# Performance work log

Measured on AMD Instinct MI355X. Metric: run time of the kernel, lower is better.

Reference implementation:

```python
import jax, jax.numpy as jnp
import numpy as np

ALPHA = 0.5        # damping from conf['alpha']
MAX_ITERS = 30     # fixed-point iterations (conf uses up to 150 with eps early-exit)
GN_GROUPS = 3
GN_EPS = 1e-5
SLOPE = 0.01       # F.leaky_relu default negative_slope


def _conv(x, w, b, pad):
    y = jax.lax.conv_general_dilated(
        x, w, window_strides=(1, 1), padding=[(pad, pad), (pad, pad)],
        dimension_numbers=("NCHW", "OIHW", "NCHW"))
    return y + b[None, :, None, None]


def _leaky(x):
    return jnp.where(x >= 0, x, SLOPE * x)


def _groupnorm(x, gamma, beta):
    N, C, H, W = x.shape
    xg = x.reshape(N, GN_GROUPS, C // GN_GROUPS, H, W)
    mu = xg.mean(axis=(2, 3, 4), keepdims=True)
    var = xg.var(axis=(2, 3, 4), keepdims=True)
    xg = (xg - mu) * jax.lax.rsqrt(var + GN_EPS)
    x = xg.reshape(N, C, H, W)
    return x * gamma[None, :, None, None] + beta[None, :, None, None]


def setup_inputs() -> dict:
    key = jax.random.key(0)
    ks = jax.random.split(key, 8)
    image = jax.random.normal(ks[0], (1024, 3, 32, 32), dtype=jnp.float32)
    # Unit params (small init keeps the fixed-point iteration contractive)
    w1 = jax.random.normal(ks[1], (6, 8, 5, 5), dtype=jnp.float32) * 0.05
    b1 = jnp.zeros((6,), jnp.float32)
    gamma = jnp.ones((6,), jnp.float32)
    beta = jnp.zeros((6,), jnp.float32)
    w2 = jax.random.normal(ks[2], (5, 6, 5, 5), dtype=jnp.float32) * 0.05
    b2 = jnp.zeros((5,), jnp.float32)
    # detection head: Conv2d(5, 10, 32, padding=0) -> full-image conv
    wh = jax.random.normal(ks[3], (10, 5, 32, 32), dtype=jnp.float32) * 0.01
    bh = jnp.zeros((10,), jnp.float32)
    return {"image": image, "w1": w1, "b1": b1, "gamma": gamma, "beta": beta,
            "w2": w2, "b2": b2, "wh": wh, "bh": bh}


def reference(image, w1, b1, gamma, beta, w2, b2, wh, bh):
    N = image.shape[0]
    z0 = jnp.zeros((N, 5, 32, 32), image.dtype)

    def unit(z):
        zx = jnp.concatenate([z, image], axis=1)
        h = _groupnorm(_leaky(_conv(zx, w1, b1, 2)), gamma, beta)
        return _leaky(_conv(h, w2, b2, 2))

    def step(z, _):
        z = (1.0 - ALPHA) * z + ALPHA * unit(z)
        return z, None

    z, _ = jax.lax.scan(step, z0, None, length=MAX_ITERS)
    return _conv(z, wh, bh, 0)
```

## Files before the change

kernel.cpp:

```cpp
#include <hip/hip_runtime.h>
#include <hip/hip_fp16.h>


typedef _Float16 half8 __attribute__((ext_vector_type(8)));
typedef float f32x4 __attribute__((ext_vector_type(4)));

#define HOFF   34
#define NBUF   (71 * 36 * 4)
#define WL1_DW 10224
#define WL2_DW 12784
#define NLDS   15344

__device__ __forceinline__ unsigned pk2(float a, float b) {
    __half2 h = __float22half2_rn(make_float2(a, b));
    return *reinterpret_cast<unsigned*>(&h);
}
__device__ __forceinline__ float2 up2(unsigned u) {
    __half2 h = *reinterpret_cast<__half2*>(&u);
    return __half22float2(h);
}
__device__ __forceinline__ unsigned hmul2(unsigned a, unsigned b) {
    __half2 r = __hmul2(*reinterpret_cast<__half2*>(&a), *reinterpret_cast<__half2*>(&b));
    return *reinterpret_cast<unsigned*>(&r);
}
__device__ __forceinline__ float lrelu(float x) { return fmaxf(x, 0.01f * x); }
__device__ __forceinline__ int swz(int x) { return (x * 16) ^ ((x & 8) << 1); }
__device__ __forceinline__ int bofs(int r, int x) { return r * 576 + swz(x); }

__global__ void pack_weights(const float* __restrict__ w1,
                             const float* __restrict__ w2,
                             unsigned* __restrict__ ws)
{
    int t = blockIdx.x * 256 + threadIdx.x;
    if (t < 640) {
        int c = t >> 6, l = t & 63;
        int row = l & 15, tg = l >> 4;
        int dx = row >> 3, oc = row & 7;
        int ty = c >> 1, tx = 4 * (c & 1) + tg, kx = tx - dx;
        unsigned q[4];
        #pragma unroll
        for (int d = 0; d < 4; ++d) {
            float v0 = 0.f, v1 = 0.f;
            if (oc < 6 && kx >= 0 && kx < 5) {
                v0 = w1[(oc * 8 + 2 * d) * 25 + ty * 5 + kx];
                v1 = w1[(oc * 8 + 2 * d + 1) * 25 + ty * 5 + kx];
            }
            q[d] = pk2(v0, v1);
        }
        *(uint4*)&ws[t * 4] = make_uint4(q[0], q[1], q[2], q[3]);
    } else if (t < 1280) {
        int u = t - 640;
        int c = u >> 6, l = u & 63;
        int row = l & 15, tg = l >> 4;
        int dx = row >> 3, oc = row & 7;
        int ty = c >> 1, tx = 4 * (c & 1) + tg, kx = tx - dx;
        unsigned q[4];
        #pragma unroll
        for (int d = 0; d < 4; ++d) {
            float v0 = 0.f, v1 = 0.f;
            if (oc < 5 && kx >= 0 && kx < 5) {
                if (2 * d < 6)     v0 = w2[(oc * 6 + 2 * d) * 25 + ty * 5 + kx];
                if (2 * d + 1 < 6) v1 = w2[(oc * 6 + 2 * d + 1) * 25 + ty * 5 + kx];
            }
            q[d] = pk2(v0, v1);
        }
        *(uint4*)&ws[2560 + u * 4] = make_uint4(q[0], q[1], q[2], q[3]);
    }
}

__global__ __launch_bounds__(256, 2)
void deq_kernel(const float* __restrict__ image,
                const unsigned* __restrict__ wks,
                const float* __restrict__ b1,
                const float* __restrict__ gam, const float* __restrict__ bet,
                const float* __restrict__ b2,
                const float* __restrict__ wh, const float* __restrict__ bh,
                float* __restrict__ out)
{
    __shared__ __align__(16) unsigned lds[NLDS];
    __shared__ float red[48];

    const int n    = blockIdx.x;
    const int tid  = threadIdx.x;
    const int lane = tid & 63;
    const int wid  = tid >> 6;
    const int col  = lane & 15;
    const int tg   = lane >> 4;
    const int dxl  = tg >> 1;
    const int sub  = tg & 1;

    for (int p = tid; p < NBUF; p += 256) lds[p] = 0u;
    for (int p = tid; p < 2560; p += 256) {
        lds[WL1_DW + p] = wks[p];
        lds[WL2_DW + p] = wks[2560 + p];
    }
    __syncthreads();

    {
        const int yy = tid >> 3, xx0 = (tid & 7) << 2;
        float4 i0 = *(const float4*)&image[(n * 3 + 0) * 1024 + yy * 32 + xx0];
        float4 i1 = *(const float4*)&image[(n * 3 + 1) * 1024 + yy * 32 + xx0];
        float4 i2 = *(const float4*)&image[(n * 3 + 2) * 1024 + yy * 32 + xx0];
        float a0[4] = {i0.x, i0.y, i0.z, i0.w};
        float a1[4] = {i1.x, i1.y, i1.z, i1.w};
        float a2[4] = {i2.x, i2.y, i2.z, i2.w};
        #pragma unroll
        for (int i = 0; i < 4; ++i) {
            unsigned* bp = (unsigned*)((char*)lds + bofs(yy + 2, xx0 + 2 + i));
            bp[2] = pk2(0.f, a0[i]);
            bp[3] = pk2(a1[i], a2[i]);
            unsigned* hp = (unsigned*)((char*)lds + bofs(yy + 2 + HOFF, xx0 + 2 + i));
            hp[3] = 0x00003C00u;
        }
    }

    int sx2[2];
    #pragma unroll
    for (int txh = 0; txh < 2; ++txh)
        sx2[txh] = swz(2 * col + 4 * txh + tg);

    float b1q[4], b2q[4];
    #pragma unroll
    for (int r = 0; r < 4; ++r) {
        int oc = (tg * 4 + r) & 7;
        b1q[r] = (oc < 6) ? b1[oc] : 0.f;
        b2q[r] = (oc < 5) ? b2[oc] : 0.f;
    }
    const f32x4 ai1 = {b1q[0], b1q[1], b1q[2], b1q[3]};
    const f32x4 ai2 = {b2q[0], b2q[1], b2q[2], b2q[3]};

    __syncthreads();

    const int ay0 = wid << 3;
    const int hwB = bofs(0, 2 * col + dxl + 2);
    const int wlo = lane << 2;

    #pragma unroll 1
    for (int it = 0; it < 30; ++it) {
        uint4 fw[10];
        #pragma unroll
        for (int c = 0; c < 10; ++c)
            fw[c] = *(const uint4*)&lds[WL1_DW + c * 256 + wlo];

        f32x4 acc[8];
        #pragma unroll
        for (int g = 0; g < 8; ++g) acc[g] = ai1;

        #pragma unroll
        for (int pr = 0; pr < 12; ++pr) {
            const char* rowp = (const char*)lds + (ay0 + pr) * 576;
            #pragma unroll
            for (int txh = 0; txh < 2; ++txh) {
                half8 pv = *(const half8*)(rowp + sx2[txh]);
                #pragma unroll
                for (int ty = 0; ty < 5; ++ty) {
                    const int g = pr - ty;
                    if (g >= 0 && g < 8)
                        acc[g] = __builtin_amdgcn_mfma_f32_16x16x32_f16(
                            __builtin_bit_cast(half8, fw[ty * 2 + txh]), pv, acc[g], 0, 0, 0);
                }
            }
        }

        float ps_lo = 0.f, ps_hi = 0.f, pq_lo = 0.f, pq_hi = 0.f;
        #pragma unroll
        for (int g = 0; g < 8; ++g) {
            float h0 = lrelu(acc[g][0]), h1 = lrelu(acc[g][1]);
            float h2 = lrelu(acc[g][2]), h3 = lrelu(acc[g][3]);
            ps_lo += h0 + h1;  pq_lo = fmaf(h0, h0, fmaf(h1, h1, pq_lo));
            ps_hi += h2 + h3;  pq_hi = fmaf(h2, h2, fmaf(h3, h3, pq_hi));
            char* wp = (char*)lds + (ay0 + g + 2 + HOFF) * 576 + (hwB - 0 * 576);
            wp = (char*)lds + bofs(ay0 + g + 2 + HOFF, 2 * col + dxl + 2);
            if (sub == 0) {
                *(uint2*)wp = make_uint2(pk2(h0, h1), pk2(h2, h3));
            } else {
                *(unsigned*)(wp + 8) = pk2(h0, h1);
            }
        }

        #pragma unroll
        for (int m = 1; m <= 8; m <<= 1) {
            ps_lo += __shfl_xor(ps_lo, m); ps_hi += __shfl_xor(ps_hi, m);
            pq_lo += __shfl_xor(pq_lo, m); pq_hi += __shfl_xor(pq_hi, m);
        }
        ps_lo += __shfl_xor(ps_lo, 32); ps_hi += __shfl_xor(ps_hi, 32);
        pq_lo += __shfl_xor(pq_lo, 32); pq_hi += __shfl_xor(pq_hi, 32);
        if (lane == 0)  { red[wid * 8 + 0] = ps_lo; red[wid * 8 + 1] = ps_hi;
                          red[wid * 8 + 4] = pq_lo; red[wid * 8 + 5] = pq_hi; }
        if (lane == 16) { red[wid * 8 + 2] = ps_lo; red[wid * 8 + 6] = pq_lo; }
        __syncthreads();

        float scv[6], shv[6];
        #pragma unroll
        for (int g3 = 0; g3 < 3; ++g3) {
            float s = 0.f, q = 0.f;
            #pragma unroll
            for (int w = 0; w < 4; ++w) { s += red[w * 8 + g3]; q += red[w * 8 + 4 + g3]; }
            float mean = s * (1.f / 2048.f);
            float var  = q * (1.f / 2048.f) - mean * mean;
            float inv  = rsqrtf(var + 1e-5f);
            #pragma unroll
            for (int k = 0; k < 2; ++k) {
                int c = 2 * g3 + k;
                scv[c] = inv * gam[c];
                shv[c] = bet[c] - mean * scv[c];
            }
        }
        unsigned sp0 = pk2(scv[0], scv[1]), sp1 = pk2(scv[2], scv[3]), sp2 = pk2(scv[4], scv[5]);

        #pragma unroll
        for (int c = 0; c < 10; ++c) {
            uint4 wr = *(const uint4*)&lds[WL2_DW + c * 256 + wlo];
            float2 a = up2(wr.x), b = up2(wr.y), cc = up2(wr.z);
            float pw = fmaf(a.x, shv[0], fmaf(a.y, shv[1],
                       fmaf(b.x, shv[2], fmaf(b.y, shv[3],
                       fmaf(cc.x, shv[4], cc.y * shv[5])))));
            fw[c].x = hmul2(wr.x, sp0);
            fw[c].y = hmul2(wr.y, sp1);
            fw[c].z = hmul2(wr.z, sp2);
            fw[c].w = pk2(pw, 0.f);
        }

        #pragma unroll
        for (int g = 0; g < 8; ++g) acc[g] = ai2;

        #pragma unroll
        for (int pr = 0; pr < 12; ++pr) {
            const char* rowp = (const char*)lds + (HOFF + ay0 + pr) * 576;
            #pragma unroll
            for (int txh = 0; txh < 2; ++txh) {
                half8 pv = *(const half8*)(rowp + sx2[txh]);
                #pragma unroll
                for (int ty = 0; ty < 5; ++ty) {
                    const int g = pr - ty;
                    if (g >= 0 && g < 8)
                        acc[g] = __builtin_amdgcn_mfma_f32_16x16x32_f16(
                            __builtin_bit_cast(half8, fw[ty * 2 + txh]), pv, acc[g], 0, 0, 0);
                }
            }
        }

        #pragma unroll
        for (int g = 0; g < 8; ++g) {
            char* zp = (char*)lds + bofs(ay0 + g + 2, 2 * col + dxl + 2);
            if (sub == 0) {
                uint2 zo = *(uint2*)zp;
                float2 za = up2(zo.x), zc = up2(zo.y);
                float z0 = 0.5f * za.x + 0.5f * lrelu(acc[g][0]);
                float z1 = 0.5f * za.y + 0.5f * lrelu(acc[g][1]);
                float z2 = 0.5f * zc.x + 0.5f * lrelu(acc[g][2]);
                float z3 = 0.5f * zc.y + 0.5f * lrelu(acc[g][3]);
                *(uint2*)zp = make_uint2(pk2(z0, z1), pk2(z2, z3));
            } else {
                _Float16* pz = (_Float16*)(zp + 8);
                float z4 = 0.5f * (float)pz[0] + 0.5f * lrelu(acc[g][0]);
                pz[0] = (_Float16)z4;
            }
        }
        __syncthreads();
    }

    {
        const int yy = tid >> 3, xx0 = (tid & 7) << 2;
        float zf[5][4];
        #pragma unroll
        for (int i = 0; i < 4; ++i) {
            const unsigned* bp = (const unsigned*)((const char*)lds + bofs(yy + 2, xx0 + 2 + i));
            float2 f0 = up2(bp[0]), fb = up2(bp[1]), fc = up2(bp[2]);
            zf[0][i] = f0.x; zf[1][i] = f0.y; zf[2][i] = fb.x; zf[3][i] = fb.y; zf[4][i] = fc.x;
        }
        float ho[10];
        #pragma unroll
        for (int o = 0; o < 10; ++o) ho[o] = 0.f;
        #pragma unroll
        for (int c = 0; c < 5; ++c) {
            #pragma unroll
            for (int o = 0; o < 10; ++o) {
                float4 wv = *(const float4*)&wh[(o * 5 + c) * 1024 + yy * 32 + xx0];
                ho[o] = fmaf(zf[c][0], wv.x, ho[o]);
                ho[o] = fmaf(zf[c][1], wv.y, ho[o]);
                ho[o] = fmaf(zf[c][2], wv.z, ho[o]);
                ho[o] = fmaf(zf[c][3], wv.w, ho[o]);
            }
        }
        #pragma unroll
        for (int m = 1; m < 64; m <<= 1) {
            #pragma unroll
            for (int o = 0; o < 10; ++o) ho[o] += __shfl_xor(ho[o], m);
        }
        if (lane == 0) {
            #pragma unroll
            for (int o = 0; o < 10; ++o) red[wid * 10 + o] = ho[o];
        }
    }
    __syncthreads();
    if (tid < 10)
        out[n * 10 + tid] = red[tid] + red[10 + tid] + red[20 + tid] + red[30 + tid] + bh[tid];
}

extern "C" void kernel_launch(void* const* d_in, const int* in_sizes, int n_in,
                              void* d_out, int out_size, void* d_ws, size_t ws_size,
                              hipStream_t stream) {
    const float* image = (const float*)d_in[0];
    const float* w1    = (const float*)d_in[1];
    const float* b1    = (const float*)d_in[2];
    const float* gam   = (const float*)d_in[3];
    const float* bet   = (const float*)d_in[4];
    const float* w2    = (const float*)d_in[5];
    const float* b2    = (const float*)d_in[6];
    const float* wh    = (const float*)d_in[7];
    const float* bh    = (const float*)d_in[8];
    float* out = (float*)d_out;
    unsigned* ws = (unsigned*)d_ws;

    pack_weights<<<5, 256, 0, stream>>>(w1, w2, ws);

    const int N = in_sizes[0] / (3 * 32 * 32);
    deq_kernel<<<N, 256, 0, stream>>>(image, ws, b1, gam, bet, b2, wh, bh, out);
}
```

Before: 335.8 us.

## Process each image with a single wavefront and keep conv weights in registers

Each image is now handled by one 64-thread wavefront instead of four, looping over four 8-row bands in series. This removes all block barriers and the shared-memory reduction for the group-norm statistics, which now use wave shuffles. Both packed conv weight sets are held in registers rather than reloaded from LDS every iteration, which also shrinks LDS per block. The trade-off is far fewer waves resident per CU, so MFMA and LDS latency are less hidden, and each image takes longer on its own.

```diff
diff --git a/kernel.cpp b/kernel.cpp
--- a/kernel.cpp
+++ b/kernel.cpp
@@ -5,11 +5,8 @@
 typedef _Float16 half8 __attribute__((ext_vector_type(8)));
 typedef float f32x4 __attribute__((ext_vector_type(4)));
 
-#define HOFF   34
-#define NBUF   (71 * 36 * 4)
-#define WL1_DW 10224
-#define WL2_DW 12784
-#define NLDS   15344
+#define HOFF 34
+#define NBUF (71 * 36 * 4)
 
 __device__ __forceinline__ unsigned pk2(float a, float b) {
     __half2 h = __float22half2_rn(make_float2(a, b));
@@ -68,7 +65,7 @@
     }
 }
 
-__global__ __launch_bounds__(256, 2)
+__global__ __launch_bounds__(64, 1)
 void deq_kernel(const float* __restrict__ image,
                 const unsigned* __restrict__ wks,
                 const float* __restrict__ b1,
@@ -77,41 +74,45 @@
                 const float* __restrict__ wh, const float* __restrict__ bh,
                 float* __restrict__ out)
 {
-    __shared__ __align__(16) unsigned lds[NLDS];
-    __shared__ float red[48];
+    __shared__ __align__(16) unsigned lds[NBUF];
 
     const int n    = blockIdx.x;
-    const int tid  = threadIdx.x;
-    const int lane = tid & 63;
-    const int wid  = tid >> 6;
+    const int lane = threadIdx.x;
     const int col  = lane & 15;
     const int tg   = lane >> 4;
     const int dxl  = tg >> 1;
     const int sub  = tg & 1;
 
-    for (int p = tid; p < NBUF; p += 256) lds[p] = 0u;
-    for (int p = tid; p < 2560; p += 256) {
-        lds[WL1_DW + p] = wks[p];
-        lds[WL2_DW + p] = wks[2560 + p];
-    }
+    for (int p = lane; p < NBUF; p += 64) lds[p] = 0u;
     __syncthreads();
 
     {
-        const int yy = tid >> 3, xx0 = (tid & 7) << 2;
-        float4 i0 = *(const float4*)&image[(n * 3 + 0) * 1024 + yy * 32 + xx0];
-        float4 i1 = *(const float4*)&image[(n * 3 + 1) * 1024 + yy * 32 + xx0];
-        float4 i2 = *(const float4*)&image[(n * 3 + 2) * 1024 + yy * 32 + xx0];
-        float a0[4] = {i0.x, i0.y, i0.z, i0.w};
-        float a1[4] = {i1.x, i1.y, i1.z, i1.w};
-        float a2[4] = {i2.x, i2.y, i2.z, i2.w};
-        #pragma unroll
-        for (int i = 0; i < 4; ++i) {
-            unsigned* bp = (unsigned*)((char*)lds + bofs(yy + 2, xx0 + 2 + i));
-            bp[2] = pk2(0.f, a0[i]);
-            bp[3] = pk2(a1[i], a2[i]);
-            unsigned* hp = (unsigned*)((char*)lds + bofs(yy + 2 + HOFF, xx0 + 2 + i));
-            hp[3] = 0x00003C00u;
-        }
+        #pragma unroll 1
+        for (int r = 0; r < 4; ++r) {
+            int t = lane + r * 64;
+            const int yy = t >> 3, xx0 = (t & 7) << 2;
+            float4 i0 = *(const float4*)&image[(n * 3 + 0) * 1024 + yy * 32 + xx0];
+            float4 i1 = *(const float4*)&image[(n * 3 + 1) * 1024 + yy * 32 + xx0];
+            float4 i2 = *(const float4*)&image[(n * 3 + 2) * 1024 + yy * 32 + xx0];
+            float a0[4] = {i0.x, i0.y, i0.z, i0.w};
+            float a1[4] = {i1.x, i1.y, i1.z, i1.w};
+            float a2[4] = {i2.x, i2.y, i2.z, i2.w};
+            #pragma unroll
+            for (int i = 0; i < 4; ++i) {
+                unsigned* bp = (unsigned*)((char*)lds + bofs(yy + 2, xx0 + 2 + i));
+                bp[2] = pk2(0.f, a0[i]);
+                bp[3] = pk2(a1[i], a2[i]);
+                unsigned* hp = (unsigned*)((char*)lds + bofs(yy + 2 + HOFF, xx0 + 2 + i));
+                hp[3] = 0x00003C00u;
+            }
+        }
+    }
+
+    uint4 f1[10], f2[10];
+    #pragma unroll
+    for (int c = 0; c < 10; ++c) {
+        f1[c] = *(const uint4*)&wks[(c * 64 + lane) * 4];
+        f2[c] = *(const uint4*)&wks[2560 + (c * 64 + lane) * 4];
     }
 
     int sx2[2];
@@ -119,62 +120,60 @@
     for (int txh = 0; txh < 2; ++txh)
         sx2[txh] = swz(2 * col + 4 * txh + tg);
 
+    const int chb = sub * 4;
     float b1q[4], b2q[4];
     #pragma unroll
     for (int r = 0; r < 4; ++r) {
-        int oc = (tg * 4 + r) & 7;
+        int oc = chb + r;
         b1q[r] = (oc < 6) ? b1[oc] : 0.f;
         b2q[r] = (oc < 5) ? b2[oc] : 0.f;
     }
     const f32x4 ai1 = {b1q[0], b1q[1], b1q[2], b1q[3]};
     const f32x4 ai2 = {b2q[0], b2q[1], b2q[2], b2q[3]};
+    float gv[6], bv[6];
+    #pragma unroll
+    for (int c = 0; c < 6; ++c) { gv[c] = gam[c]; bv[c] = bet[c]; }
 
     __syncthreads();
 
-    const int ay0 = wid << 3;
-    const int hwB = bofs(0, 2 * col + dxl + 2);
-    const int wlo = lane << 2;
+    const int hwx = swz(2 * col + dxl + 2);
 
     #pragma unroll 1
     for (int it = 0; it < 30; ++it) {
-        uint4 fw[10];
-        #pragma unroll
-        for (int c = 0; c < 10; ++c)
-            fw[c] = *(const uint4*)&lds[WL1_DW + c * 256 + wlo];
-
-        f32x4 acc[8];
-        #pragma unroll
-        for (int g = 0; g < 8; ++g) acc[g] = ai1;
-
-        #pragma unroll
-        for (int pr = 0; pr < 12; ++pr) {
-            const char* rowp = (const char*)lds + (ay0 + pr) * 576;
-            #pragma unroll
-            for (int txh = 0; txh < 2; ++txh) {
-                half8 pv = *(const half8*)(rowp + sx2[txh]);
+        float ps_lo = 0.f, ps_hi = 0.f, pq_lo = 0.f, pq_hi = 0.f;
+        #pragma unroll 1
+        for (int b = 0; b < 4; ++b) {
+            const int ay = b << 3;
+            f32x4 acc[8];
+            #pragma unroll
+            for (int g = 0; g < 8; ++g) acc[g] = ai1;
+            #pragma unroll
+            for (int pr = 0; pr < 12; ++pr) {
+                const char* rowp = (const char*)lds + (ay + pr) * 576;
                 #pragma unroll
-                for (int ty = 0; ty < 5; ++ty) {
-                    const int g = pr - ty;
-                    if (g >= 0 && g < 8)
-                        acc[g] = __builtin_amdgcn_mfma_f32_16x16x32_f16(
-                            __builtin_bit_cast(half8, fw[ty * 2 + txh]), pv, acc[g], 0, 0, 0);
-                }
-            }
-        }
-
-        float ps_lo = 0.f, ps_hi = 0.f, pq_lo = 0.f, pq_hi = 0.f;
-        #pragma unroll
-        for (int g = 0; g < 8; ++g) {
-            float h0 = lrelu(acc[g][0]), h1 = lrelu(acc[g][1]);
-            float h2 = lrelu(acc[g][2]), h3 = lrelu(acc[g][3]);
-            ps_lo += h0 + h1;  pq_lo = fmaf(h0, h0, fmaf(h1, h1, pq_lo));
-            ps_hi += h2 + h3;  pq_hi = fmaf(h2, h2, fmaf(h3, h3, pq_hi));
-            char* wp = (char*)lds + (ay0 + g + 2 + HOFF) * 576 + (hwB - 0 * 576);
-            wp = (char*)lds + bofs(ay0 + g + 2 + HOFF, 2 * col + dxl + 2);
-            if (sub == 0) {
-                *(uint2*)wp = make_uint2(pk2(h0, h1), pk2(h2, h3));
-            } else {
-                *(unsigned*)(wp + 8) = pk2(h0, h1);
+                for (int txh = 0; txh < 2; ++txh) {
+                    half8 pv = *(const half8*)(rowp + sx2[txh]);
+                    #pragma unroll
+                    for (int ty = 0; ty < 5; ++ty) {
+                        const int g = pr - ty;
+                        if (g >= 0 && g < 8)
+                            acc[g] = __builtin_amdgcn_mfma_f32_16x16x32_f16(
+                                __builtin_bit_cast(half8, f1[ty * 2 + txh]), pv, acc[g], 0, 0, 0);
+                    }
+                }
+            }
+            #pragma unroll
+            for (int g = 0; g < 8; ++g) {
+                float h0 = lrelu(acc[g][0]), h1 = lrelu(acc[g][1]);
+                float h2 = lrelu(acc[g][2]), h3 = lrelu(acc[g][3]);
+                ps_lo += h0 + h1;  pq_lo = fmaf(h0, h0, fmaf(h1, h1, pq_lo));
+                ps_hi += h2 + h3;  pq_hi = fmaf(h2, h2, fmaf(h3, h3, pq_hi));
+                char* wp = (char*)lds + (ay + g + 2 + HOFF) * 576 + hwx;
+                if (sub == 0) {
+                    *(uint2*)wp = make_uint2(pk2(h0, h1), pk2(h2, h3));
+                } else {
+                    *(unsigned*)(wp + 8) = pk2(h0, h1);
+                }
             }
         }
 
@@ -185,102 +184,105 @@
         }
         ps_lo += __shfl_xor(ps_lo, 32); ps_hi += __shfl_xor(ps_hi, 32);
         pq_lo += __shfl_xor(pq_lo, 32); pq_hi += __shfl_xor(pq_hi, 32);
-        if (lane == 0)  { red[wid * 8 + 0] = ps_lo; red[wid * 8 + 1] = ps_hi;
-                          red[wid * 8 + 4] = pq_lo; red[wid * 8 + 5] = pq_hi; }
-        if (lane == 16) { red[wid * 8 + 2] = ps_lo; red[wid * 8 + 6] = pq_lo; }
-        __syncthreads();
+        float sg[3], qg[3];
+        sg[0] = __shfl(ps_lo, 0);  qg[0] = __shfl(pq_lo, 0);
+        sg[1] = __shfl(ps_hi, 0);  qg[1] = __shfl(pq_hi, 0);
+        sg[2] = __shfl(ps_lo, 16); qg[2] = __shfl(pq_lo, 16);
 
         float scv[6], shv[6];
         #pragma unroll
         for (int g3 = 0; g3 < 3; ++g3) {
-            float s = 0.f, q = 0.f;
-            #pragma unroll
-            for (int w = 0; w < 4; ++w) { s += red[w * 8 + g3]; q += red[w * 8 + 4 + g3]; }
-            float mean = s * (1.f / 2048.f);
-            float var  = q * (1.f / 2048.f) - mean * mean;
+            float mean = sg[g3] * (1.f / 2048.f);
+            float var  = qg[g3] * (1.f / 2048.f) - mean * mean;
             float inv  = rsqrtf(var + 1e-5f);
             #pragma unroll
             for (int k = 0; k < 2; ++k) {
                 int c = 2 * g3 + k;
-                scv[c] = inv * gam[c];
-                shv[c] = bet[c] - mean * scv[c];
+                scv[c] = inv * gv[c];
+                shv[c] = bv[c] - mean * scv[c];
             }
         }
         unsigned sp0 = pk2(scv[0], scv[1]), sp1 = pk2(scv[2], scv[3]), sp2 = pk2(scv[4], scv[5]);
 
+        uint4 fw[10];
         #pragma unroll
         for (int c = 0; c < 10; ++c) {
-            uint4 wr = *(const uint4*)&lds[WL2_DW + c * 256 + wlo];
-            float2 a = up2(wr.x), b = up2(wr.y), cc = up2(wr.z);
+            float2 a = up2(f2[c].x), bb = up2(f2[c].y), cc = up2(f2[c].z);
             float pw = fmaf(a.x, shv[0], fmaf(a.y, shv[1],
-                       fmaf(b.x, shv[2], fmaf(b.y, shv[3],
+                       fmaf(bb.x, shv[2], fmaf(bb.y, shv[3],
                        fmaf(cc.x, shv[4], cc.y * shv[5])))));
-            fw[c].x = hmul2(wr.x, sp0);
-            fw[c].y = hmul2(wr.y, sp1);
-            fw[c].z = hmul2(wr.z, sp2);
+            fw[c].x = hmul2(f2[c].x, sp0);
+            fw[c].y = hmul2(f2[c].y, sp1);
+            fw[c].z = hmul2(f2[c].z, sp2);
             fw[c].w = pk2(pw, 0.f);
         }
 
-        #pragma unroll
-        for (int g = 0; g < 8; ++g) acc[g] = ai2;
-
-        #pragma unroll
-        for (int pr = 0; pr < 12; ++pr) {
-            const char* rowp = (const char*)lds + (HOFF + ay0 + pr) * 576;
-            #pragma unroll
-            for (int txh = 0; txh < 2; ++txh) {
-                half8 pv = *(const half8*)(rowp + sx2[txh]);
+        #pragma unroll 1
+        for (int b = 0; b < 4; ++b) {
+            const int ay = b << 3;
+            f32x4 acc[8];
+            #pragma unroll
+            for (int g = 0; g < 8; ++g) acc[g] = ai2;
+            #pragma unroll
+            for (int pr = 0; pr < 12; ++pr) {
+                const char* rowp = (const char*)lds + (HOFF + ay + pr) * 576;
                 #pragma unroll
-                for (int ty = 0; ty < 5; ++ty) {
-                    const int g = pr - ty;
-                    if (g >= 0 && g < 8)
-                        acc[g] = __builtin_amdgcn_mfma_f32_16x16x32_f16(
-                            __builtin_bit_cast(half8, fw[ty * 2 + txh]), pv, acc[g], 0, 0, 0);
-                }
-            }
-        }
-
-        #pragma unroll
-        for (int g = 0; g < 8; ++g) {
-            char* zp = (char*)lds + bofs(ay0 + g + 2, 2 * col + dxl + 2);
-            if (sub == 0) {
-                uint2 zo = *(uint2*)zp;
-                float2 za = up2(zo.x), zc = up2(zo.y);
-                float z0 = 0.5f * za.x + 0.5f * lrelu(acc[g][0]);
-                float z1 = 0.5f * za.y + 0.5f * lrelu(acc[g][1]);
-                float z2 = 0.5f * zc.x + 0.5f * lrelu(acc[g][2]);
-                float z3 = 0.5f * zc.y + 0.5f * lrelu(acc[g][3]);
-                *(uint2*)zp = make_uint2(pk2(z0, z1), pk2(z2, z3));
-            } else {
-                _Float16* pz = (_Float16*)(zp + 8);
-                float z4 = 0.5f * (float)pz[0] + 0.5f * lrelu(acc[g][0]);
-                pz[0] = (_Float16)z4;
-            }
-        }
-        __syncthreads();
+                for (int txh = 0; txh < 2; ++txh) {
+                    half8 pv = *(const half8*)(rowp + sx2[txh]);
+                    #pragma unroll
+                    for (int ty = 0; ty < 5; ++ty) {
+                        const int g = pr - ty;
+                        if (g >= 0 && g < 8)
+                            acc[g] = __builtin_amdgcn_mfma_f32_16x16x32_f16(
+                                __builtin_bit_cast(half8, fw[ty * 2 + txh]), pv, acc[g], 0, 0, 0);
+                    }
+                }
+            }
+            #pragma unroll
+            for (int g = 0; g < 8; ++g) {
+                char* zp = (char*)lds + (ay + g + 2) * 576 + hwx;
+                if (sub == 0) {
+                    uint2 zo = *(uint2*)zp;
+                    float2 za = up2(zo.x), zc = up2(zo.y);
+                    float z0 = 0.5f * za.x + 0.5f * lrelu(acc[g][0]);
+                    float z1 = 0.5f * za.y + 0.5f * lrelu(acc[g][1]);
+                    float z2 = 0.5f * zc.x + 0.5f * lrelu(acc[g][2]);
+                    float z3 = 0.5f * zc.y + 0.5f * lrelu(acc[g][3]);
+                    *(uint2*)zp = make_uint2(pk2(z0, z1), pk2(z2, z3));
+                } else {
+                    _Float16* pz = (_Float16*)(zp + 8);
+                    float z4 = 0.5f * (float)pz[0] + 0.5f * lrelu(acc[g][0]);
+                    pz[0] = (_Float16)z4;
+                }
+            }
+        }
     }
 
     {
-        const int yy = tid >> 3, xx0 = (tid & 7) << 2;
-        float zf[5][4];
-        #pragma unroll
-        for (int i = 0; i < 4; ++i) {
-            const unsigned* bp = (const unsigned*)((const char*)lds + bofs(yy + 2, xx0 + 2 + i));
-            float2 f0 = up2(bp[0]), fb = up2(bp[1]), fc = up2(bp[2]);
-            zf[0][i] = f0.x; zf[1][i] = f0.y; zf[2][i] = fb.x; zf[3][i] = fb.y; zf[4][i] = fc.x;
-        }
         float ho[10];
         #pragma unroll
         for (int o = 0; o < 10; ++o) ho[o] = 0.f;
-        #pragma unroll
-        for (int c = 0; c < 5; ++c) {
-            #pragma unroll
-            for (int o = 0; o < 10; ++o) {
-                float4 wv = *(const float4*)&wh[(o * 5 + c) * 1024 + yy * 32 + xx0];
-                ho[o] = fmaf(zf[c][0], wv.x, ho[o]);
-                ho[o] = fmaf(zf[c][1], wv.y, ho[o]);
-                ho[o] = fmaf(zf[c][2], wv.z, ho[o]);
-                ho[o] = fmaf(zf[c][3], wv.w, ho[o]);
+        #pragma unroll 1
+        for (int r = 0; r < 4; ++r) {
+            int grp = lane + r * 64;
+            const int yy = grp >> 3, xx0 = (grp & 7) << 2;
+            float zf[5][4];
+            #pragma unroll
+            for (int i = 0; i < 4; ++i) {
+                const unsigned* bp = (const unsigned*)((const char*)lds + bofs(yy + 2, xx0 + 2 + i));
+                float2 f0 = up2(bp[0]), fb = up2(bp[1]), fc = up2(bp[2]);
+                zf[0][i] = f0.x; zf[1][i] = f0.y; zf[2][i] = fb.x; zf[3][i] = fb.y; zf[4][i] = fc.x;
+            }
+            #pragma unroll
+            for (int c = 0; c < 5; ++c) {
+                #pragma unroll
+                for (int o = 0; o < 10; ++o) {
+                    float4 wv = *(const float4*)&wh[(o * 5 + c) * 1024 + yy * 32 + xx0];
+                    ho[o] = fmaf(zf[c][0], wv.x, ho[o]);
+                    ho[o] = fmaf(zf[c][1], wv.y, ho[o]);
+                    ho[o] = fmaf(zf[c][2], wv.z, ho[o]);
+                    ho[o] = fmaf(zf[c][3], wv.w, ho[o]);
+                }
             }
         }
         #pragma unroll
@@ -288,14 +290,9 @@
             #pragma unroll
             for (int o = 0; o < 10; ++o) ho[o] += __shfl_xor(ho[o], m);
         }
-        if (lane == 0) {
-            #pragma unroll
-            for (int o = 0; o < 10; ++o) red[wid * 10 + o] = ho[o];
-        }
-    }
-    __syncthreads();
-    if (tid < 10)
-        out[n * 10 + tid] = red[tid] + red[10 + tid] + red[20 + tid] + red[30 + tid] + bh[tid];
+        if (lane < 10)
+            out[n * 10 + lane] = ho[lane] + bh[lane];
+    }
 }
 
 extern "C" void kernel_launch(void* const* d_in, const int* in_sizes, int n_in,
@@ -316,5 +313,5 @@
     pack_weights<<<5, 256, 0, stream>>>(w1, w2, ws);
 
     const int N = in_sizes[0] / (3 * 32 * 32);
-    deq_kernel<<<N, 256, 0, stream>>>(image, ws, b1, gam, bet, b2, wh, bh, out);
-}
+    deq_kernel<<<N, 64, 0, stream>>>(image, ws, b1, gam, bet, b2, wh, bh, out);
+}
```

Measured after the change: 400.8 us. +19.4%, slower.
